# Kernel optimization log

Measured on AMD Instinct MI355X. Metric: run time of the kernel, lower is better.

Reference implementation:

```python
import jax, jax.numpy as jnp
import numpy as np

B, C, D, T = 64, 1024, 32, 32
F4 = C // 4
GLOBAL_MARGIN = 0.2
MAX_VIOLATION = True
EPS = 1e-8


def setup_inputs() -> dict:
    key = jax.random.key(0)
    k = jax.random.split(key, 8)
    videos = jax.random.normal(k[0], (B, C, D, T), jnp.float32)
    sentences = jax.random.normal(k[1], (B, C), jnp.float32)
    lam = jnp.full((1,), 0.3, jnp.float32)
    mask = jnp.ones((B, D, T), jnp.int32)
    iou_maps = jax.random.uniform(k[2], (D * T, D * T), dtype=jnp.float32)
    lim = float(np.sqrt(6.0 / (C + F4)))  # xavier_uniform for Linear(C, C//4)
    W_v = jax.random.uniform(k[3], (4, C, F4), jnp.float32, -lim, lim)
    b_v = jnp.zeros((4, F4), jnp.float32)
    W_s = jax.random.uniform(k[4], (4, C, F4), jnp.float32, -lim, lim)
    b_s = jnp.zeros((4, F4), jnp.float32)
    return dict(videos=videos, sentences=sentences, lam=lam, mask=mask,
                iou_maps=iou_maps, valid_num=50,
                W_v=W_v, b_v=b_v, W_s=W_s, b_s=b_s)


def _forward(videos, sentences, W_v, b_v, W_s, b_s, lam, mask, iou_maps, valid_num):
    b, c, d, t = videos.shape
    # per-sample channel-mean centering
    videos = videos - jnp.mean(videos, axis=1, keepdims=True)
    sentences = sentences - jnp.mean(sentences, axis=1, keepdims=True)
    # 4-way linear projections, concatenated back along channel dim
    v = jnp.transpose(videos, (0, 2, 3, 1))                      # [b,d,t,c]
    v_cat = (jnp.einsum('bdtc,kcf->bkfdt', v, W_v)
             + b_v[None, :, :, None, None]).reshape(b, c, d, t)  # [b,c,d,t]
    s_cat = (jnp.einsum('bc,kcf->bkf', sentences, W_s) + b_s[None]).reshape(b, c)
    # cosine similarity over channel dim, vectorized over the batch loop
    vn = v_cat / jnp.maximum(jnp.linalg.norm(v_cat, axis=1, keepdims=True), EPS)
    sn = s_cat / jnp.maximum(jnp.linalg.norm(s_cat, axis=1, keepdims=True), EPS)
    sim = jnp.einsum('bcdt,sc->sbdt', vn, sn)                    # [s,b,d,t]
    sim = jnp.where(mask[None] == 0, -jnp.inf, sim)
    positive_map = sim[jnp.arange(b), jnp.arange(b)]             # [b,d,t]
    # top-k proposals + soft-NMS suppression (get_video_score_nms)
    flat = sim.reshape(b, b, d * t)
    vals, idx = jax.lax.top_k(flat, valid_num)                   # [s,b,v]
    iou_sub = iou_maps[idx[..., :, None], idx[..., None, :]]     # [s,b,v,v]
    tril = jnp.tril(jnp.ones((valid_num, valid_num), vals.dtype), -1)
    penalty = jnp.einsum('sblk,lk->sbk', iou_sub * iou_sub, tril)
    w = jnp.exp(-penalty / lam[0])                               # gaussian soft-NMS weight
    scores = jnp.mean(vals * w, axis=-1)                         # [s,b]
    # margin-based contrastive loss on the b x b score matrix
    diag = jnp.diagonal(scores)
    cost_s = jnp.clip(GLOBAL_MARGIN + scores - diag[:, None], 0.0)
    cost_im = jnp.clip(GLOBAL_MARGIN + scores - diag[None, :], 0.0)
    eye = jnp.eye(b, dtype=bool)
    cost_s = jnp.where(eye, 0.0, cost_s)
    cost_im = jnp.where(eye, 0.0, cost_im)
    if MAX_VIOLATION:
        cost_s = cost_s.max(axis=1)
        cost_im = cost_im.max(axis=0)
    loss = cost_s.sum() / b + cost_im.sum() / b
    return loss, positive_map


def reference(videos, sentences, lam, mask, iou_maps, valid_num, W_v, b_v, W_s, b_s):
    return _forward(videos, sentences, W_v, b_v, W_s, b_s, lam, mask, iou_maps, valid_num)
```

## Files before the change

kernel.cpp:

```cpp
#include <hip/hip_runtime.h>
#include <cstdint>
#include <cstddef>

#define CDIM  1024
#define DTDIM 1024
#define MDIM  65536
#define BDIM  64
#define VNUM  50

typedef __attribute__((ext_vector_type(8))) short bf16x8;
typedef __attribute__((ext_vector_type(4))) float f32x4;

__device__ __forceinline__ float bf2f(unsigned int u16) {
  return __uint_as_float(u16 << 16);
}
__device__ __forceinline__ unsigned short f2bf(float x) {
  unsigned int u = __float_as_uint(x);
  u += 0x7fffu + ((u >> 16) & 1u);
  return (unsigned short)(u >> 16);
}

__device__ __forceinline__ void gload16(const void* g, void* l) {
  __builtin_amdgcn_global_load_lds((const __attribute__((address_space(1))) void*)g,
                                   (__attribute__((address_space(3))) void*)l,
                                   16, 0, 0);
}

__global__ void k_transpose_videos(const float* __restrict__ vid,
                                   unsigned short* __restrict__ At,
                                   float* __restrict__ vsums) {
  __shared__ float t[64][65];
  const int tid = threadIdx.x;
  const int dt0 = blockIdx.x * 64, c0 = blockIdx.y * 64, b = blockIdx.z;
  const int lc = tid >> 4;
  const int l4 = (tid & 15) * 4;
  const float* src = vid + ((size_t)b * CDIM + c0) * DTDIM + dt0;
#pragma unroll
  for (int p = 0; p < 4; p++) {
    const int c = p * 16 + lc;
    const float4 f = *reinterpret_cast<const float4*>(&src[(size_t)c * DTDIM + l4]);
    t[c][l4 + 0] = f.x; t[c][l4 + 1] = f.y; t[c][l4 + 2] = f.z; t[c][l4 + 3] = f.w;
  }
  __syncthreads();
  const int dr = tid >> 5;
  const int cl = tid & 31;
  unsigned int* dstbase = reinterpret_cast<unsigned int*>(
      At + ((size_t)(b * DTDIM + dt0)) * CDIM + c0);
#pragma unroll
  for (int p = 0; p < 8; p++) {
    const int dt = p * 8 + dr;
    const float a0 = t[2 * cl][dt], a1 = t[2 * cl + 1][dt];
    const unsigned int u = (unsigned int)f2bf(a0) | ((unsigned int)f2bf(a1) << 16);
    dstbase[(size_t)dt * 512 + cl] = u;
    float s = a0 + a1;
    s += __shfl_xor(s, 1);  s += __shfl_xor(s, 2);  s += __shfl_xor(s, 4);
    s += __shfl_xor(s, 8);  s += __shfl_xor(s, 16);
    if (cl == 0) atomicAdd(&vsums[(size_t)b * DTDIM + dt0 + dt], s);
  }
}

__global__ void k_transpose_W(const float* __restrict__ W,
                              unsigned short* __restrict__ Wt) {
  __shared__ float t[32][33];
  const int tx = threadIdx.x & 31, ty = threadIdx.x >> 5;
  const int f0 = blockIdx.x * 32, c0 = blockIdx.y * 32, kb = blockIdx.z;
  const float* src = W + ((size_t)kb * CDIM + c0) * 256 + f0;
#pragma unroll
  for (int i = 0; i < 4; i++) {
    const int cl = ty + i * 8;
    t[cl][tx] = src[(size_t)cl * 256 + tx];
  }
  __syncthreads();
  unsigned short* dst = Wt + ((size_t)(kb * 256 + f0)) * CDIM + c0;
#pragma unroll
  for (int i = 0; i < 4; i++) {
    const int fl = ty + i * 8;
    dst[(size_t)fl * CDIM + tx] = f2bf(t[tx][fl]);
  }
}

__global__ void k_row_sums(const unsigned short* __restrict__ A,
                           float* __restrict__ out, int nrows) {
  const int wave = threadIdx.x >> 6, lane = threadIdx.x & 63;
  const int row = blockIdx.x * 4 + wave;
  if (row >= nrows) return;
  const unsigned short* r = A + (size_t)row * 1024;
  float s = 0.f;
#pragma unroll
  for (int h = 0; h < 2; h++) {
    const uint4 u = *reinterpret_cast<const uint4*>(r + h * 512 + lane * 8);
    s += bf2f(u.x & 0xffffu) + bf2f(u.x >> 16);
    s += bf2f(u.y & 0xffffu) + bf2f(u.y >> 16);
    s += bf2f(u.z & 0xffffu) + bf2f(u.z >> 16);
    s += bf2f(u.w & 0xffffu) + bf2f(u.w >> 16);
  }
#pragma unroll
  for (int o = 32; o; o >>= 1) s += __shfl_down(s, o);
  if (lane == 0) out[row] = s;
}

__global__ void k_scat(const float* __restrict__ sent, const float* __restrict__ Ws,
                       const float* __restrict__ bs, unsigned short* __restrict__ scat,
                       float* __restrict__ snorm2) {
  const int s = blockIdx.x, j = blockIdx.y, tid = threadIdx.x;
  __shared__ float sc[1024];
  __shared__ float red[4];
  float p = 0.f;
#pragma unroll
  for (int q = 0; q < 4; q++) {
    const float x = sent[(size_t)s * 1024 + tid + q * 256];
    sc[tid + q * 256] = x;
    p += x;
  }
#pragma unroll
  for (int o = 32; o; o >>= 1) p += __shfl_down(p, o);
  const int wave = tid >> 6, lane = tid & 63;
  if (lane == 0) red[wave] = p;
  __syncthreads();
  const float mean = (red[0] + red[1] + red[2] + red[3]) * (1.f / 1024.f);
  float acc = 0.f;
  const float* W = Ws + ((size_t)j * 1024) * 256 + tid;
  for (int c = 0; c < 1024; c++) acc += (sc[c] - mean) * W[(size_t)c * 256];
  const int n = j * 256 + tid;
  const float val = acc + bs[n];
  scat[(size_t)s * 1024 + n] = f2bf(val);
  float v2 = val * val;
#pragma unroll
  for (int o = 32; o; o >>= 1) v2 += __shfl_down(v2, o);
  if (lane == 0) atomicAdd(&snorm2[s], v2);
}

__global__ __launch_bounds__(512, 2) void k_gemm_fused(
    const unsigned short* __restrict__ At, const unsigned short* __restrict__ Wt,
    const float* __restrict__ vsums, const float* __restrict__ csW,
    const float* __restrict__ bv, const unsigned short* __restrict__ scat,
    const float* __restrict__ snorm2, const int* __restrict__ mask,
    float* __restrict__ sim, float* __restrict__ pm) {
  __shared__ alignas(16) char smem[116992];
  unsigned short* sA    = (unsigned short*)smem;
  unsigned short* sB    = (unsigned short*)(smem + 65536);
  unsigned short* stile = (unsigned short*)(smem + 98304);
  float* invSnLds       = (float*)(smem + 114688);
  float* vnLds          = (float*)(smem + 114944);
  unsigned short* vtile = (unsigned short*)smem;

  const int tid = threadIdx.x;
  const int wave = tid >> 6, lane = tid & 63;
  const int quad = lane >> 4, l16 = lane & 15;
  const int m0 = blockIdx.x * 256;
  const int wm = (wave & 3) * 64, wn = (wave >> 2) * 64;
  const int r8 = lane >> 3, g8 = lane & 7;

  if (tid < 64) invSnLds[tid] = 1.f / fmaxf(sqrtf(snorm2[tid]), 1e-8f);

  f32x4 acc2[4][2];
#pragma unroll
  for (int i = 0; i < 4; i++)
#pragma unroll
    for (int j = 0; j < 2; j++) acc2[i][j] = f32x4{0.f, 0.f, 0.f, 0.f};
  float ss[4][4];
#pragma unroll
  for (int i = 0; i < 4; i++)
#pragma unroll
    for (int rr = 0; rr < 4; rr++) ss[i][rr] = 0.f;

  const float inv1024 = 1.f / 1024.f;

#pragma unroll 1
  for (int nt = 0; nt < 8; ++nt) {
    const int n0 = nt * 128;

    auto stage_ab = [&](int buf, int kt) {
      const int koff = kt * 64;
      unsigned short* dA = sA + buf * 16384;
      unsigned short* dB = sB + buf * 8192;
#pragma unroll
      for (int ii = 0; ii < 4; ii++) {
        const int q = ii * 8 + wave;
        const int r = q * 8 + r8;
        gload16(At + (size_t)(m0 + r) * CDIM + koff + (g8 ^ r8) * 8, dA + q * 512);
      }
#pragma unroll
      for (int ii = 0; ii < 2; ii++) {
        const int q = ii * 8 + wave;
        const int r = q * 8 + r8;
        gload16(Wt + (size_t)(n0 + r) * CDIM + koff + (g8 ^ r8) * 8, dB + q * 512);
      }
    };

    f32x4 acc[4][4];
#pragma unroll
    for (int i = 0; i < 4; i++)
#pragma unroll
      for (int j = 0; j < 4; j++) acc[i][j] = f32x4{0.f, 0.f, 0.f, 0.f};

    auto compute = [&](int buf) {
      const unsigned short* bA = sA + buf * 16384;
      const unsigned short* bB = sB + buf * 8192;
      __builtin_amdgcn_s_setprio(1);
#pragma unroll
      for (int ks = 0; ks < 2; ks++) {
        const int slot = ((ks * 4 + quad) ^ (l16 & 7)) * 8;
        bf16x8 aF[4], bF[4];
#pragma unroll
        for (int i = 0; i < 4; i++)
          aF[i] = *reinterpret_cast<const bf16x8*>(&bA[(wm + i * 16 + l16) * 64 + slot]);
#pragma unroll
        for (int j = 0; j < 4; j++)
          bF[j] = *reinterpret_cast<const bf16x8*>(&bB[(wn + j * 16 + l16) * 64 + slot]);
#pragma unroll
        for (int i = 0; i < 4; i++)
#pragma unroll
          for (int j = 0; j < 4; j++)
            acc[i][j] = __builtin_amdgcn_mfma_f32_16x16x32_bf16(aF[i], bF[j], acc[i][j], 0, 0, 0);
      }
      __builtin_amdgcn_s_setprio(0);
    };

#pragma unroll
    for (int ii = 0; ii < 2; ii++) {
      const int q = ii * 8 + wave;
      const int srow = q * 4 + (lane >> 4);
      const int g = (lane & 15) ^ (srow & 15);
      gload16(scat + (size_t)srow * 1024 + n0 + g * 8, stile + q * 512);
    }
    stage_ab(0, 0);

    int cur = 0;
#pragma unroll 1
    for (int kt = 0; kt < 15; ++kt) {
      stage_ab(cur ^ 1, kt + 1);
      asm volatile("s_waitcnt vmcnt(6)" ::: "memory");
      __builtin_amdgcn_s_barrier();
      asm volatile("" ::: "memory");
      compute(cur);
      __builtin_amdgcn_s_barrier();
      cur ^= 1;
    }
    asm volatile("s_waitcnt vmcnt(0)" ::: "memory");
    __builtin_amdgcn_s_barrier();
    asm volatile("" ::: "memory");
    compute(cur);
    __syncthreads();

#pragma unroll
    for (int i = 0; i < 4; i++) {
      const int rbase = wm + i * 16 + quad * 4;
      const float4 vs = *reinterpret_cast<const float4*>(&vsums[m0 + rbase]);
      const float mu[4] = {vs.x * inv1024, vs.y * inv1024, vs.z * inv1024, vs.w * inv1024};
#pragma unroll
      for (int j = 0; j < 4; j++) {
        const int c = wn + j * 16 + l16;
        const float cs = csW[n0 + c];
        const float bb = bv[n0 + c];
#pragma unroll
        for (int rr = 0; rr < 4; rr++) {
          const int m = rbase + rr;
          const float val = acc[i][j][rr] - mu[rr] * cs + bb;
          ss[i][rr] += val * val;
          const int slot = (c >> 3) ^ (m & 15);
          vtile[m * 128 + slot * 8 + (c & 7)] = f2bf(val);
        }
      }
    }
    __syncthreads();

#pragma unroll
    for (int ks2 = 0; ks2 < 4; ks2++) {
      const int slot = ((ks2 * 4 + quad) ^ l16) * 8;
      bf16x8 a2[4], b2[2];
#pragma unroll
      for (int i2 = 0; i2 < 4; i2++)
        a2[i2] = *reinterpret_cast<const bf16x8*>(&stile[(i2 * 16 + l16) * 128 + slot]);
#pragma unroll
      for (int j2 = 0; j2 < 2; j2++)
        b2[j2] = *reinterpret_cast<const bf16x8*>(&vtile[(wave * 32 + j2 * 16 + l16) * 128 + slot]);
#pragma unroll
      for (int i2 = 0; i2 < 4; i2++)
#pragma unroll
        for (int j2 = 0; j2 < 2; j2++)
          acc2[i2][j2] = __builtin_amdgcn_mfma_f32_16x16x32_bf16(a2[i2], b2[j2], acc2[i2][j2], 0, 0, 0);
    }
    __syncthreads();
  }

#pragma unroll
  for (int i = 0; i < 4; i++)
#pragma unroll
    for (int rr = 0; rr < 4; rr++) {
      float v = ss[i][rr];
      v += __shfl_xor(v, 1); v += __shfl_xor(v, 2);
      v += __shfl_xor(v, 4); v += __shfl_xor(v, 8);
      if (l16 == 0) vnLds[(wave >> 2) * 256 + wm + i * 16 + quad * 4 + rr] = v;
    }
  __syncthreads();

  const int b0 = m0 >> 10;
#pragma unroll
  for (int j2 = 0; j2 < 2; j2++) {
    const int ml = wave * 32 + j2 * 16 + l16;
    const float nv = vnLds[ml] + vnLds[256 + ml];
    const float invVn = 1.f / fmaxf(sqrtf(nv), 1e-8f);
    const int mk = mask[m0 + ml];
#pragma unroll
    for (int i2 = 0; i2 < 4; i2++) {
#pragma unroll
      for (int reg = 0; reg < 4; reg++) {
        const int s = i2 * 16 + quad * 4 + reg;
        float val = acc2[i2][j2][reg] * invVn * invSnLds[s];
        if (mk == 0) val = -__builtin_inff();
        sim[(size_t)s * MDIM + m0 + ml] = val;
        if (s == b0) pm[m0 + ml] = val;
      }
    }
  }
}

__global__ void k_topk(const float* __restrict__ sim, const float* __restrict__ iou,
                       const float* __restrict__ lam, float* __restrict__ scores) {
  const int wave = threadIdx.x >> 6, lane = threadIdx.x & 63;
  const int sb = blockIdx.x * 4 + wave;
  const int s = sb >> 6, b = sb & 63;
  __shared__ float tvs[4][VNUM];
  __shared__ int tis[4][VNUM];

  const float* row = sim + (size_t)s * MDIM + (size_t)b * 1024;
  float v[16];
#pragma unroll
  for (int j = 0; j < 16; j++) v[j] = row[j * 64 + lane];

  for (int k = 0; k < VNUM; k++) {
    float bv = v[0]; int bj = 0;
#pragma unroll
    for (int j = 1; j < 16; j++)
      if (v[j] > bv) { bv = v[j]; bj = j; }
    int bidx = bj * 64 + lane;
#pragma unroll
    for (int o = 1; o < 64; o <<= 1) {
      const float ov = __shfl_xor(bv, o);
      const int oi = __shfl_xor(bidx, o);
      if (ov > bv || (ov == bv && oi < bidx)) { bv = ov; bidx = oi; }
    }
    if (lane == 0) { tvs[wave][k] = bv; tis[wave][k] = bidx; }
    const int wj = bidx >> 6;
    const bool mine = (bidx & 63) == lane;
#pragma unroll
    for (int j = 0; j < 16; j++)
      if (mine && wj == j) v[j] = -__builtin_inff();
  }
  __syncthreads();

  float contrib = 0.f;
  if (lane < VNUM) {
    const int myidx = tis[wave][lane];
    float pen = 0.f;
    for (int l = lane + 1; l < VNUM; l++) {
      const float u = iou[(size_t)tis[wave][l] * 1024 + myidx];
      pen += u * u;
    }
    contrib = tvs[wave][lane] * expf(-pen / lam[0]);
  }
#pragma unroll
  for (int o = 32; o; o >>= 1) contrib += __shfl_down(contrib, o);
  if (lane == 0) scores[s * 64 + b] = contrib * (1.f / VNUM);
}

__global__ void k_loss(const float* __restrict__ scores, float* __restrict__ out) {
  __shared__ float S[64 * 64];
  __shared__ float diag[64];
  __shared__ float rmax[64], cmax[64];
  const int tid = threadIdx.x;
#pragma unroll
  for (int q = 0; q < 16; q++) S[tid + q * 256] = scores[tid + q * 256];
  __syncthreads();
  if (tid < 64) diag[tid] = S[tid * 64 + tid];
  __syncthreads();
  if (tid < 64) {
    float rm = 0.f, cm = 0.f;
    for (int x = 0; x < 64; x++) {
      if (x != tid) {
        const float cs = 0.2f + S[tid * 64 + x] - diag[tid];
        rm = fmaxf(rm, fmaxf(cs, 0.f));
        const float ci = 0.2f + S[x * 64 + tid] - diag[tid];
        cm = fmaxf(cm, fmaxf(ci, 0.f));
      }
    }
    rmax[tid] = rm; cmax[tid] = cm;
  }
  __syncthreads();
  if (tid == 0) {
    float L = 0.f;
    for (int t = 0; t < 64; t++) L += rmax[t] + cmax[t];
    out[0] = L * (1.f / 64.f);
  }
}

extern "C" void kernel_launch(void* const* d_in, const int* in_sizes, int n_in,
                              void* d_out, int out_size, void* d_ws, size_t ws_size,
                              hipStream_t stream) {
  (void)in_sizes; (void)n_in; (void)out_size; (void)ws_size;
  const float* videos = (const float*)d_in[0];
  const float* sent   = (const float*)d_in[1];
  const float* lam    = (const float*)d_in[2];
  const int*   mask   = (const int*)d_in[3];
  const float* iou    = (const float*)d_in[4];
  const float* W_v    = (const float*)d_in[6];
  const float* b_v    = (const float*)d_in[7];
  const float* W_s    = (const float*)d_in[8];
  const float* b_s    = (const float*)d_in[9];
  float* out = (float*)d_out;

  char* ws = (char*)d_ws;
  unsigned short* At   = (unsigned short*)(ws + 0);
  float* sim           = (float*)(ws + 134217728);
  unsigned short* Wt   = (unsigned short*)(ws + 150994944);
  unsigned short* scat = (unsigned short*)(ws + 153092096);
  float* vsums         = (float*)(ws + 153223168);
  float* snorm2        = (float*)(ws + 153485312);
  float* csW           = (float*)(ws + 153485568);
  float* scores        = (float*)(ws + 153489664);

  hipMemsetAsync(vsums, 0, 262144 + 256, stream);

  k_transpose_videos<<<dim3(16, 16, 64), 256, 0, stream>>>(videos, At, vsums);
  k_transpose_W<<<dim3(8, 32, 4), 256, 0, stream>>>(W_v, Wt);
  k_row_sums<<<256, 256, 0, stream>>>(Wt, csW, 1024);
  k_scat<<<dim3(64, 4), 256, 0, stream>>>(sent, W_s, b_s, scat, snorm2);
  k_gemm_fused<<<dim3(256), 512, 0, stream>>>(At, Wt, vsums, csW, b_v, scat,
                                              snorm2, mask, sim, out + 1);
  k_topk<<<dim3(1024), 256, 0, stream>>>(sim, iou, lam, scores);
  k_loss<<<1, 256, 0, stream>>>(scores, out);
}
```

Baseline: 717.8 us.

## Retile fused GEMM to full-N row blocks, replace atomics, widen sentence projection

The fused projection GEMM now gives each block 64 rows against the full 1024-column weight, with a K-step of 32. This removes the outer loop over eight column tiles and the repeated A reloads, and it raises the grid from 256 to 1024 blocks. The second similarity GEMM then runs over eight staged sentence chunks after the whole projected tile sits in LDS. Video channel sums move from atomics to per-tile partials reduced by a separate kernel. The sentence projection uses 1024 threads that split the channel loop four ways. Shared memory grows to about 157KB, which limits each CU to one block, and vpart reuses the sim workspace buffer.

```diff
diff --git a/kernel.cpp b/kernel.cpp
--- a/kernel.cpp
+++ b/kernel.cpp
@@ -28,7 +28,7 @@
 
 __global__ void k_transpose_videos(const float* __restrict__ vid,
                                    unsigned short* __restrict__ At,
-                                   float* __restrict__ vsums) {
+                                   float* __restrict__ vpart) {
   __shared__ float t[64][65];
   const int tid = threadIdx.x;
   const int dt0 = blockIdx.x * 64, c0 = blockIdx.y * 64, b = blockIdx.z;
@@ -55,8 +55,18 @@
     float s = a0 + a1;
     s += __shfl_xor(s, 1);  s += __shfl_xor(s, 2);  s += __shfl_xor(s, 4);
     s += __shfl_xor(s, 8);  s += __shfl_xor(s, 16);
-    if (cl == 0) atomicAdd(&vsums[(size_t)b * DTDIM + dt0 + dt], s);
-  }
+    if (cl == 0)
+      vpart[(size_t)blockIdx.y * MDIM + (size_t)b * DTDIM + dt0 + dt] = s;
+  }
+}
+
+__global__ void k_vsum_reduce(const float* __restrict__ vpart,
+                              float* __restrict__ vsums) {
+  const int i = blockIdx.x * 256 + threadIdx.x;
+  float s = 0.f;
+#pragma unroll
+  for (int ct = 0; ct < 16; ct++) s += vpart[(size_t)ct * MDIM + i];
+  vsums[i] = s;
 }
 
 __global__ void k_transpose_W(const float* __restrict__ W,
@@ -104,30 +114,36 @@
                        float* __restrict__ snorm2) {
   const int s = blockIdx.x, j = blockIdx.y, tid = threadIdx.x;
   __shared__ float sc[1024];
-  __shared__ float red[4];
-  float p = 0.f;
-#pragma unroll
-  for (int q = 0; q < 4; q++) {
-    const float x = sent[(size_t)s * 1024 + tid + q * 256];
-    sc[tid + q * 256] = x;
-    p += x;
-  }
+  __shared__ float red[16];
+  __shared__ float part[4][256];
+  const float x = sent[(size_t)s * 1024 + tid];
+  sc[tid] = x;
+  float p = x;
 #pragma unroll
   for (int o = 32; o; o >>= 1) p += __shfl_down(p, o);
-  const int wave = tid >> 6, lane = tid & 63;
-  if (lane == 0) red[wave] = p;
-  __syncthreads();
-  const float mean = (red[0] + red[1] + red[2] + red[3]) * (1.f / 1024.f);
+  if ((tid & 63) == 0) red[tid >> 6] = p;
+  __syncthreads();
+  float mean = 0.f;
+#pragma unroll
+  for (int w = 0; w < 16; w++) mean += red[w];
+  mean *= (1.f / 1024.f);
+  const int f = tid & 255, cq = tid >> 8;
+  const float* W = Ws + ((size_t)(j * 1024 + cq * 256)) * 256 + f;
   float acc = 0.f;
-  const float* W = Ws + ((size_t)j * 1024) * 256 + tid;
-  for (int c = 0; c < 1024; c++) acc += (sc[c] - mean) * W[(size_t)c * 256];
-  const int n = j * 256 + tid;
-  const float val = acc + bs[n];
-  scat[(size_t)s * 1024 + n] = f2bf(val);
-  float v2 = val * val;
-#pragma unroll
-  for (int o = 32; o; o >>= 1) v2 += __shfl_down(v2, o);
-  if (lane == 0) atomicAdd(&snorm2[s], v2);
+#pragma unroll 8
+  for (int c = 0; c < 256; c++)
+    acc += (sc[cq * 256 + c] - mean) * W[(size_t)c * 256];
+  part[cq][f] = acc;
+  __syncthreads();
+  if (tid < 256) {
+    const int n = j * 256 + tid;
+    const float val = part[0][tid] + part[1][tid] + part[2][tid] + part[3][tid] + bs[n];
+    scat[(size_t)s * 1024 + n] = f2bf(val);
+    float v2 = val * val;
+#pragma unroll
+    for (int o = 32; o; o >>= 1) v2 += __shfl_down(v2, o);
+    if ((tid & 63) == 0) atomicAdd(&snorm2[s], v2);
+  }
 }
 
 __global__ __launch_bounds__(512, 2) void k_gemm_fused(
@@ -136,182 +152,186 @@
     const float* __restrict__ bv, const unsigned short* __restrict__ scat,
     const float* __restrict__ snorm2, const int* __restrict__ mask,
     float* __restrict__ sim, float* __restrict__ pm) {
-  __shared__ alignas(16) char smem[116992];
+  __shared__ alignas(16) char smem[157184];
   unsigned short* sA    = (unsigned short*)smem;
-  unsigned short* sB    = (unsigned short*)(smem + 65536);
-  unsigned short* stile = (unsigned short*)(smem + 98304);
-  float* invSnLds       = (float*)(smem + 114688);
-  float* vnLds          = (float*)(smem + 114944);
+  unsigned short* sB    = (unsigned short*)(smem + 8192);
+  unsigned short* stile = (unsigned short*)(smem + 139264);
+  float* invSnLds       = (float*)(smem + 155648);
+  float* vnLds          = (float*)(smem + 155904);
+  float* invVnLds       = (float*)(smem + 156928);
   unsigned short* vtile = (unsigned short*)smem;
 
   const int tid = threadIdx.x;
   const int wave = tid >> 6, lane = tid & 63;
   const int quad = lane >> 4, l16 = lane & 15;
-  const int m0 = blockIdx.x * 256;
-  const int wm = (wave & 3) * 64, wn = (wave >> 2) * 64;
-  const int r8 = lane >> 3, g8 = lane & 7;
+  const int m0 = blockIdx.x * 64;
+  const int mg = wave >> 2, ng = wave & 3;
+  const int r4 = lane >> 2, c4 = lane & 3;
 
   if (tid < 64) invSnLds[tid] = 1.f / fmaxf(sqrtf(snorm2[tid]), 1e-8f);
 
-  f32x4 acc2[4][2];
-#pragma unroll
-  for (int i = 0; i < 4; i++)
-#pragma unroll
-    for (int j = 0; j < 2; j++) acc2[i][j] = f32x4{0.f, 0.f, 0.f, 0.f};
-  float ss[4][4];
-#pragma unroll
-  for (int i = 0; i < 4; i++)
-#pragma unroll
-    for (int rr = 0; rr < 4; rr++) ss[i][rr] = 0.f;
-
-  const float inv1024 = 1.f / 1024.f;
-
-#pragma unroll 1
-  for (int nt = 0; nt < 8; ++nt) {
-    const int n0 = nt * 128;
-
-    auto stage_ab = [&](int buf, int kt) {
-      const int koff = kt * 64;
-      unsigned short* dA = sA + buf * 16384;
-      unsigned short* dB = sB + buf * 8192;
-#pragma unroll
-      for (int ii = 0; ii < 4; ii++) {
-        const int q = ii * 8 + wave;
-        const int r = q * 8 + r8;
-        gload16(At + (size_t)(m0 + r) * CDIM + koff + (g8 ^ r8) * 8, dA + q * 512);
-      }
-#pragma unroll
-      for (int ii = 0; ii < 2; ii++) {
-        const int q = ii * 8 + wave;
-        const int r = q * 8 + r8;
-        gload16(Wt + (size_t)(n0 + r) * CDIM + koff + (g8 ^ r8) * 8, dB + q * 512);
-      }
-    };
-
-    f32x4 acc[4][4];
-#pragma unroll
-    for (int i = 0; i < 4; i++)
-#pragma unroll
-      for (int j = 0; j < 4; j++) acc[i][j] = f32x4{0.f, 0.f, 0.f, 0.f};
-
-    auto compute = [&](int buf) {
-      const unsigned short* bA = sA + buf * 16384;
-      const unsigned short* bB = sB + buf * 8192;
-      __builtin_amdgcn_s_setprio(1);
-#pragma unroll
-      for (int ks = 0; ks < 2; ks++) {
-        const int slot = ((ks * 4 + quad) ^ (l16 & 7)) * 8;
-        bf16x8 aF[4], bF[4];
-#pragma unroll
-        for (int i = 0; i < 4; i++)
-          aF[i] = *reinterpret_cast<const bf16x8*>(&bA[(wm + i * 16 + l16) * 64 + slot]);
-#pragma unroll
-        for (int j = 0; j < 4; j++)
-          bF[j] = *reinterpret_cast<const bf16x8*>(&bB[(wn + j * 16 + l16) * 64 + slot]);
-#pragma unroll
-        for (int i = 0; i < 4; i++)
-#pragma unroll
-          for (int j = 0; j < 4; j++)
-            acc[i][j] = __builtin_amdgcn_mfma_f32_16x16x32_bf16(aF[i], bF[j], acc[i][j], 0, 0, 0);
-      }
-      __builtin_amdgcn_s_setprio(0);
-    };
-
+  f32x4 acc[2][16];
+#pragma unroll
+  for (int i = 0; i < 2; i++)
+#pragma unroll
+    for (int j = 0; j < 16; j++) acc[i][j] = f32x4{0.f, 0.f, 0.f, 0.f};
+
+  auto stage_ab = [&](int buf, int kt) {
+    const int koff = kt * 32;
+    unsigned short* dB = sB + buf * 32768;
+#pragma unroll
+    for (int ii = 0; ii < 8; ii++) {
+      const int qq = wave * 8 + ii;
+      const int r = qq * 16 + r4;
+      gload16(Wt + (size_t)r * CDIM + koff + ((c4 ^ (r4 & 3)) * 8), dB + qq * 512);
+    }
+    if (wave < 4) {
+      const int r = wave * 16 + r4;
+      gload16(At + (size_t)(m0 + r) * CDIM + koff + ((c4 ^ (r4 & 3)) * 8),
+              sA + buf * 2048 + wave * 512);
+    }
+  };
+
+  auto stage_stile = [&](int cc) {
 #pragma unroll
     for (int ii = 0; ii < 2; ii++) {
       const int q = ii * 8 + wave;
       const int srow = q * 4 + (lane >> 4);
       const int g = (lane & 15) ^ (srow & 15);
-      gload16(scat + (size_t)srow * 1024 + n0 + g * 8, stile + q * 512);
-    }
-    stage_ab(0, 0);
-
-    int cur = 0;
+      gload16(scat + (size_t)srow * 1024 + cc * 128 + g * 8, stile + q * 512);
+    }
+  };
+
+  auto compute = [&](int buf) {
+    const unsigned short* bA = sA + buf * 2048;
+    const unsigned short* bB = sB + buf * 32768;
+    const int sl = (quad ^ (l16 & 3)) * 8;
+    bf16x8 aF[2];
+#pragma unroll
+    for (int i = 0; i < 2; i++)
+      aF[i] = *reinterpret_cast<const bf16x8*>(&bA[(mg * 32 + i * 16 + l16) * 32 + sl]);
+    __builtin_amdgcn_s_setprio(1);
+#pragma unroll
+    for (int jb = 0; jb < 4; jb++) {
+      bf16x8 bF[4];
+#pragma unroll
+      for (int jj = 0; jj < 4; jj++)
+        bF[jj] = *reinterpret_cast<const bf16x8*>(
+            &bB[(ng * 256 + (jb * 4 + jj) * 16 + l16) * 32 + sl]);
+#pragma unroll
+      for (int i = 0; i < 2; i++)
+#pragma unroll
+        for (int jj = 0; jj < 4; jj++)
+          acc[i][jb * 4 + jj] = __builtin_amdgcn_mfma_f32_16x16x32_bf16(
+              aF[i], bF[jj], acc[i][jb * 4 + jj], 0, 0, 0);
+    }
+    __builtin_amdgcn_s_setprio(0);
+    asm volatile("s_waitcnt lgkmcnt(0)" ::: "memory");
+    __builtin_amdgcn_sched_barrier(0);
+  };
+
+  stage_ab(0, 0);
+  int cur = 0;
 #pragma unroll 1
-    for (int kt = 0; kt < 15; ++kt) {
-      stage_ab(cur ^ 1, kt + 1);
-      asm volatile("s_waitcnt vmcnt(6)" ::: "memory");
-      __builtin_amdgcn_s_barrier();
-      asm volatile("" ::: "memory");
-      compute(cur);
-      __builtin_amdgcn_s_barrier();
-      cur ^= 1;
-    }
-    asm volatile("s_waitcnt vmcnt(0)" ::: "memory");
+  for (int kt = 0; kt < 31; ++kt) {
+    stage_ab(cur ^ 1, kt + 1);
+    if (wave < 4) asm volatile("s_waitcnt vmcnt(9)" ::: "memory");
+    else          asm volatile("s_waitcnt vmcnt(8)" ::: "memory");
     __builtin_amdgcn_s_barrier();
     asm volatile("" ::: "memory");
     compute(cur);
-    __syncthreads();
-
-#pragma unroll
-    for (int i = 0; i < 4; i++) {
-      const int rbase = wm + i * 16 + quad * 4;
-      const float4 vs = *reinterpret_cast<const float4*>(&vsums[m0 + rbase]);
-      const float mu[4] = {vs.x * inv1024, vs.y * inv1024, vs.z * inv1024, vs.w * inv1024};
-#pragma unroll
-      for (int j = 0; j < 4; j++) {
-        const int c = wn + j * 16 + l16;
-        const float cs = csW[n0 + c];
-        const float bb = bv[n0 + c];
-#pragma unroll
-        for (int rr = 0; rr < 4; rr++) {
-          const int m = rbase + rr;
-          const float val = acc[i][j][rr] - mu[rr] * cs + bb;
-          ss[i][rr] += val * val;
-          const int slot = (c >> 3) ^ (m & 15);
-          vtile[m * 128 + slot * 8 + (c & 7)] = f2bf(val);
-        }
+    __builtin_amdgcn_s_barrier();
+    cur ^= 1;
+  }
+  stage_stile(0);
+  asm volatile("s_waitcnt vmcnt(0)" ::: "memory");
+  __builtin_amdgcn_s_barrier();
+  asm volatile("" ::: "memory");
+  compute(cur);
+  __syncthreads();
+
+  const float inv1024 = 1.f / 1024.f;
+  float ss[2][4];
+#pragma unroll
+  for (int i = 0; i < 2; i++)
+#pragma unroll
+    for (int rr = 0; rr < 4; rr++) ss[i][rr] = 0.f;
+#pragma unroll
+  for (int i = 0; i < 2; i++) {
+    const int rbase = mg * 32 + i * 16 + quad * 4;
+    const float4 vs = *reinterpret_cast<const float4*>(&vsums[m0 + rbase]);
+    const float mu[4] = {vs.x * inv1024, vs.y * inv1024, vs.z * inv1024, vs.w * inv1024};
+#pragma unroll
+    for (int j = 0; j < 16; j++) {
+      const int c = ng * 256 + j * 16 + l16;
+      const float cs = csW[c];
+      const float bb = bv[c];
+#pragma unroll
+      for (int rr = 0; rr < 4; rr++) {
+        const int m = rbase + rr;
+        const float val = acc[i][j][rr] - mu[rr] * cs + bb;
+        ss[i][rr] += val * val;
+        vtile[m * 1024 + (((c >> 3) ^ (m & 15)) * 8) + (c & 7)] = f2bf(val);
       }
     }
-    __syncthreads();
-
-#pragma unroll
-    for (int ks2 = 0; ks2 < 4; ks2++) {
-      const int slot = ((ks2 * 4 + quad) ^ l16) * 8;
-      bf16x8 a2[4], b2[2];
-#pragma unroll
-      for (int i2 = 0; i2 < 4; i2++)
-        a2[i2] = *reinterpret_cast<const bf16x8*>(&stile[(i2 * 16 + l16) * 128 + slot]);
-#pragma unroll
-      for (int j2 = 0; j2 < 2; j2++)
-        b2[j2] = *reinterpret_cast<const bf16x8*>(&vtile[(wave * 32 + j2 * 16 + l16) * 128 + slot]);
-#pragma unroll
-      for (int i2 = 0; i2 < 4; i2++)
-#pragma unroll
-        for (int j2 = 0; j2 < 2; j2++)
-          acc2[i2][j2] = __builtin_amdgcn_mfma_f32_16x16x32_bf16(a2[i2], b2[j2], acc2[i2][j2], 0, 0, 0);
-    }
-    __syncthreads();
-  }
-
-#pragma unroll
-  for (int i = 0; i < 4; i++)
+  }
+
+#pragma unroll
+  for (int i = 0; i < 2; i++)
 #pragma unroll
     for (int rr = 0; rr < 4; rr++) {
       float v = ss[i][rr];
       v += __shfl_xor(v, 1); v += __shfl_xor(v, 2);
       v += __shfl_xor(v, 4); v += __shfl_xor(v, 8);
-      if (l16 == 0) vnLds[(wave >> 2) * 256 + wm + i * 16 + quad * 4 + rr] = v;
-    }
-  __syncthreads();
+      if (l16 == 0) vnLds[ng * 64 + mg * 32 + i * 16 + quad * 4 + rr] = v;
+    }
+  __syncthreads();
+  if (tid < 64) {
+    const float nv = vnLds[tid] + vnLds[64 + tid] + vnLds[128 + tid] + vnLds[192 + tid];
+    invVnLds[tid] = 1.f / fmaxf(sqrtf(nv), 1e-8f);
+  }
+
+  const int sgrp = wave >> 2, mgrp = wave & 3;
+  f32x4 acc2[2];
+#pragma unroll
+  for (int i2 = 0; i2 < 2; i2++) acc2[i2] = f32x4{0.f, 0.f, 0.f, 0.f};
+#pragma unroll 1
+  for (int cc = 0; cc < 8; cc++) {
+    if (cc > 0) {
+      __syncthreads();
+      stage_stile(cc);
+      asm volatile("s_waitcnt vmcnt(0)" ::: "memory");
+    }
+    __syncthreads();
+#pragma unroll
+    for (int ks2 = 0; ks2 < 4; ks2++) {
+      const int sl2 = ((ks2 * 4 + quad) ^ l16) * 8;
+      bf16x8 a2[2], b2;
+#pragma unroll
+      for (int i2 = 0; i2 < 2; i2++)
+        a2[i2] = *reinterpret_cast<const bf16x8*>(
+            &stile[(sgrp * 32 + i2 * 16 + l16) * 128 + sl2]);
+      b2 = *reinterpret_cast<const bf16x8*>(
+          &vtile[(mgrp * 16 + l16) * 1024 + cc * 128 + sl2]);
+#pragma unroll
+      for (int i2 = 0; i2 < 2; i2++)
+        acc2[i2] = __builtin_amdgcn_mfma_f32_16x16x32_bf16(a2[i2], b2, acc2[i2], 0, 0, 0);
+    }
+  }
 
   const int b0 = m0 >> 10;
-#pragma unroll
-  for (int j2 = 0; j2 < 2; j2++) {
-    const int ml = wave * 32 + j2 * 16 + l16;
-    const float nv = vnLds[ml] + vnLds[256 + ml];
-    const float invVn = 1.f / fmaxf(sqrtf(nv), 1e-8f);
-    const int mk = mask[m0 + ml];
-#pragma unroll
-    for (int i2 = 0; i2 < 4; i2++) {
-#pragma unroll
-      for (int reg = 0; reg < 4; reg++) {
-        const int s = i2 * 16 + quad * 4 + reg;
-        float val = acc2[i2][j2][reg] * invVn * invSnLds[s];
-        if (mk == 0) val = -__builtin_inff();
-        sim[(size_t)s * MDIM + m0 + ml] = val;
-        if (s == b0) pm[m0 + ml] = val;
-      }
+  const int m = mgrp * 16 + l16;
+  const float invVn = invVnLds[m];
+  const int mk = mask[m0 + m];
+#pragma unroll
+  for (int i2 = 0; i2 < 2; i2++) {
+#pragma unroll
+    for (int reg = 0; reg < 4; reg++) {
+      const int s = sgrp * 32 + i2 * 16 + quad * 4 + reg;
+      float val = acc2[i2][reg] * invVn * invSnLds[s];
+      if (mk == 0) val = -__builtin_inff();
+      sim[(size_t)s * MDIM + m0 + m] = val;
+      if (s == b0) pm[m0 + m] = val;
     }
   }
 }
@@ -413,6 +433,7 @@
   char* ws = (char*)d_ws;
   unsigned short* At   = (unsigned short*)(ws + 0);
   float* sim           = (float*)(ws + 134217728);
+  float* vpart         = (float*)(ws + 134217728);
   unsigned short* Wt   = (unsigned short*)(ws + 150994944);
   unsigned short* scat = (unsigned short*)(ws + 153092096);
   float* vsums         = (float*)(ws + 153223168);
@@ -420,14 +441,15 @@
   float* csW           = (float*)(ws + 153485568);
   float* scores        = (float*)(ws + 153489664);
 
-  hipMemsetAsync(vsums, 0, 262144 + 256, stream);
-
-  k_transpose_videos<<<dim3(16, 16, 64), 256, 0, stream>>>(videos, At, vsums);
+  hipMemsetAsync(snorm2, 0, 256, stream);
+
+  k_transpose_videos<<<dim3(16, 16, 64), 256, 0, stream>>>(videos, At, vpart);
+  k_vsum_reduce<<<256, 256, 0, stream>>>(vpart, vsums);
   k_transpose_W<<<dim3(8, 32, 4), 256, 0, stream>>>(W_v, Wt);
   k_row_sums<<<256, 256, 0, stream>>>(Wt, csW, 1024);
-  k_scat<<<dim3(64, 4), 256, 0, stream>>>(sent, W_s, b_s, scat, snorm2);
-  k_gemm_fused<<<dim3(256), 512, 0, stream>>>(At, Wt, vsums, csW, b_v, scat,
-                                              snorm2, mask, sim, out + 1);
+  k_scat<<<dim3(64, 4), 1024, 0, stream>>>(sent, W_s, b_s, scat, snorm2);
+  k_gemm_fused<<<dim3(1024), 512, 0, stream>>>(At, Wt, vsums, csW, b_v, scat,
+                                               snorm2, mask, sim, out + 1);
   k_topk<<<dim3(1024), 256, 0, stream>>>(sim, iou, lam, scores);
   k_loss<<<1, 256, 0, stream>>>(scores, out);
 }
```

Result: slower. 743.2 us (+3.6%).
